# Optimization experiments

Measured on AMD Instinct MI355X. Metric: run time of the kernel, lower is better.

The kernel has to match this reference:

```python
import jax, jax.numpy as jnp
import numpy as np

B, S, H, E, V, T = 64, 256, 1024, 512, 10000, 64
D = H // 2  # per-direction LSTM hidden


def setup_inputs() -> dict:
    key = jax.random.key(0)
    ks = jax.random.split(key, 16)
    s = jnp.float32(0.02)
    emb = jax.random.normal(ks[4], (V, E), jnp.float32) * s
    emb = emb.at[0].set(0.0)  # padding_idx=0
    return {
        "encoder_outputs": jax.random.normal(ks[0], (B, S, H), jnp.float32),
        "enc_h0": jax.random.normal(ks[1], (2, B, D), jnp.float32),
        "enc_c0": jax.random.normal(ks[2], (2, B, D), jnp.float32),
        "target": jax.random.randint(ks[3], (B, T), 1, V),
        "mask": jnp.zeros((B, S), jnp.bool_),
        "sos_idx": 1,
        "emb": emb,
        "Wa": jax.random.normal(ks[5], (H, H), jnp.float32) * s,
        "Ua": jax.random.normal(ks[6], (H, H), jnp.float32) * s,
        "Va": jax.random.normal(ks[7], (H,), jnp.float32) * s,
        "out_W": jax.random.normal(ks[8], (V, H), jnp.float32) * s,
        "out_b": jnp.zeros((V,), jnp.float32),
        "Wih_f": jax.random.normal(ks[9], (4 * D, E + H), jnp.float32) * s,
        "Whh_f": jax.random.normal(ks[10], (4 * D, D), jnp.float32) * s,
        "bih_f": jnp.zeros((4 * D,), jnp.float32),
        "bhh_f": jnp.zeros((4 * D,), jnp.float32),
        "Wih_b": jax.random.normal(ks[11], (4 * D, E + H), jnp.float32) * s,
        "Whh_b": jax.random.normal(ks[12], (4 * D, D), jnp.float32) * s,
        "bih_b": jnp.zeros((4 * D,), jnp.float32),
        "bhh_b": jnp.zeros((4 * D,), jnp.float32),
    }


def _lstm_cell(x, h, c, Wih, Whh, bih, bhh):
    g = x @ Wih.T + h @ Whh.T + bih + bhh
    i, f, gg, o = jnp.split(g, 4, axis=-1)  # torch gate order i,f,g,o
    c2 = jax.nn.sigmoid(f) * c + jax.nn.sigmoid(i) * jnp.tanh(gg)
    h2 = jax.nn.sigmoid(o) * jnp.tanh(c2)
    return h2, c2


def reference(encoder_outputs, enc_h0, enc_c0, target, mask, sos_idx, emb, Wa, Ua, Va,
              out_W, out_b, Wih_f, Whh_f, bih_f, bhh_f, Wih_b, Whh_b, bih_b, bhh_b):
    # Cache Ua(keys) once (original recomputes it each step; math identical).
    Uk = jnp.einsum('bsh,kh->bsk', encoder_outputs, Ua)  # [B,S,H]
    b = encoder_outputs.shape[0]
    tokens = jnp.concatenate(
        [jnp.full((b, 1), sos_idx, target.dtype), target[:, :-1]], axis=1)  # [B,T]
    xs = tokens.T  # [T,B]

    def step(carry, tok):
        h, c = carry  # each [2,B,D]
        query = jnp.swapaxes(h, 0, 1).reshape(b, -1)  # [B,H] (fwd||bwd)
        sc = jnp.einsum('bsh,h->bs', jnp.tanh((query @ Wa.T)[:, None, :] + Uk), Va)
        sc = jnp.where(mask, -jnp.inf, sc)
        w = jax.nn.softmax(sc, axis=-1)  # [B,S]
        ctx = jnp.einsum('bs,bsh->bh', w, encoder_outputs)  # [B,H]
        x = jnp.concatenate([emb[tok], ctx], axis=-1)  # [B,E+H]
        hf, cf = _lstm_cell(x, h[0], c[0], Wih_f, Whh_f, bih_f, bhh_f)
        hb, cb = _lstm_cell(x, h[1], c[1], Wih_b, Whh_b, bih_b, bhh_b)
        out = jnp.concatenate([hf, hb], axis=-1)  # [B,H]
        logits = out @ out_W.T + out_b  # [B,V]
        return (jnp.stack([hf, hb]), jnp.stack([cf, cb])), (logits, w)

    (h, c), (logits, attns) = jax.lax.scan(step, (enc_h0, enc_c0), xs)
    decoder_outputs = jnp.swapaxes(logits, 0, 1)  # [B,T,V]
    attentions = jnp.swapaxes(attns, 0, 1)        # [B,T,S]
    return decoder_outputs, h, c, attentions
```

## Files before the change

kernel.cpp:

```cpp
#include <hip/hip_runtime.h>

#define NB 64
#define NS 256
#define NH 1024
#define NE 512
#define NV 10000
#define NT 64
#define ND 512
#define NEH 1536

typedef __attribute__((ext_vector_type(8))) short bf16x8;
typedef __attribute__((ext_vector_type(4))) float f32x4;

__device__ __forceinline__ short F2B(float f) {
  unsigned u = __float_as_uint(f);
  return (short)((u + 0x7fffu + ((u >> 16) & 1u)) >> 16);
}
__device__ __forceinline__ float B2F(short s) {
  return __uint_as_float(((unsigned)(unsigned short)s) << 16);
}
__device__ __forceinline__ float ftanh(float x) {
  float e = __expf(2.f * x);
  return 1.f - 2.f * __builtin_amdgcn_rcpf(e + 1.f);
}

#define GLD16(src, dst)                                                        \
  __builtin_amdgcn_global_load_lds(                                            \
      (const __attribute__((address_space(1))) void*)(src),                    \
      (__attribute__((address_space(3))) void*)(dst), 16, 0, 0)

__device__ __forceinline__ void mm64_f32a(
    const float* __restrict__ Af, int lda, const short* __restrict__ Wg,
    int ldw, int K, short* Ch, size_t ldc, char* smem)
{
  const int tid = threadIdx.x;
  const int lane = tid & 63, w = tid >> 6;
  const int qm = (w >> 1) << 5, qn = (w & 1) << 5;
  const int kg = lane >> 4, rl = lane & 15;
  f32x4 acc[2][2] = {};
  const int nIt = K >> 6;

  auto stage = [&](int k0, int buf) {
    char* As = smem + (buf << 14);
    char* Bs = As + 8192;
#pragma unroll
    for (int p = 0; p < 2; ++p) {
      int j = tid + (p << 8);
      int row = j >> 3;
      int c = (j & 7) ^ (row & 7);
      const float* src = Af + (size_t)row * lda + k0 + (c << 3);
      float4 v0 = ((const float4*)src)[0];
      float4 v1 = ((const float4*)src)[1];
      bf16x8 pk;
      pk[0] = F2B(v0.x); pk[1] = F2B(v0.y); pk[2] = F2B(v0.z); pk[3] = F2B(v0.w);
      pk[4] = F2B(v1.x); pk[5] = F2B(v1.y); pk[6] = F2B(v1.z); pk[7] = F2B(v1.w);
      *((bf16x8*)As + j) = pk;
    }
#pragma unroll
    for (int p = 0; p < 2; ++p) {
      int j = (w << 7) + (p << 6) + lane;
      int row = j >> 3;
      int c = (j & 7) ^ (row & 7);
      GLD16(Wg + (size_t)row * ldw + k0 + (c << 3), Bs + (w << 11) + (p << 10));
    }
  };

  stage(0, 0);
  for (int it = 0; it < nIt; ++it) {
    __syncthreads();
    if (it + 1 < nIt) stage((it + 1) << 6, (it + 1) & 1);
    const short* As = (const short*)(smem + ((it & 1) << 14));
    const short* Bs = As + 4096;
#pragma unroll
    for (int kk = 0; kk < 2; ++kk) {
      bf16x8 af[2], bfr[2];
#pragma unroll
      for (int mt = 0; mt < 2; ++mt) {
        int r2 = qm + (mt << 4) + rl;
        int c = (kk << 2) + kg;
        af[mt] = *((const bf16x8*)As + ((r2 << 3) | (c ^ (r2 & 7))));
      }
#pragma unroll
      for (int nt = 0; nt < 2; ++nt) {
        int r2 = qn + (nt << 4) + rl;
        int c = (kk << 2) + kg;
        bfr[nt] = *((const bf16x8*)Bs + ((r2 << 3) | (c ^ (r2 & 7))));
      }
#pragma unroll
      for (int mt = 0; mt < 2; ++mt)
#pragma unroll
        for (int nt = 0; nt < 2; ++nt)
          acc[mt][nt] = __builtin_amdgcn_mfma_f32_16x16x32_bf16(
              af[mt], bfr[nt], acc[mt][nt], 0, 0, 0);
    }
  }
#pragma unroll
  for (int mt = 0; mt < 2; ++mt)
#pragma unroll
    for (int nt = 0; nt < 2; ++nt) {
      int cn = qn + (nt << 4) + rl;
#pragma unroll
      for (int r = 0; r < 4; ++r) {
        int rowm = qm + (mt << 4) + (kg << 2) + r;
        Ch[(size_t)rowm * ldc + cn] = F2B(acc[mt][nt][r]);
      }
    }
}

__global__ __launch_bounds__(256) void uk_mm_f32(const float* __restrict__ enc,
                                                 const short* __restrict__ Ua_h,
                                                 short* __restrict__ Uk_h) {
  __shared__ char smem[32768];
  mm64_f32a(enc + (size_t)blockIdx.y * 64 * NH, NH,
            Ua_h + (size_t)blockIdx.x * 64 * NH, NH, NH,
            Uk_h + (size_t)blockIdx.y * 64 * NH + blockIdx.x * 64, NH, smem);
}

template <int MODE>
__global__ __launch_bounds__(256) void mm128(
    const short* __restrict__ A, const short* __restrict__ Bw, int nvmax,
    const float* __restrict__ bias, float* __restrict__ Cf,
    short* __restrict__ Ch)
{
  __shared__ char smem[32768];
  const int tid = threadIdx.x, lane = tid & 63, w = tid >> 6;
  const int m0 = blockIdx.y << 7;
  const int n0 = blockIdx.x << 7;
  const int qm = (w >> 1) << 6, qn = (w & 1) << 6;
  const int kg = lane >> 4, rl = lane & 15;
  f32x4 acc[4][4] = {};
  for (int k0 = 0; k0 < NH; k0 += 64) {
#pragma unroll
    for (int p = 0; p < 4; ++p) {
      int j = (((w << 2) + p) << 6) + lane;
      int row = j >> 3;
      int c = (j & 7) ^ (row & 7);
      GLD16(A + (size_t)(m0 + row) * NH + k0 + (c << 3),
            smem + (((w << 2) + p) << 10));
      int vr = n0 + row; if (vr > nvmax - 1) vr = nvmax - 1;
      GLD16(Bw + (size_t)vr * NH + k0 + (c << 3),
            smem + 16384 + (((w << 2) + p) << 10));
    }
    __syncthreads();
    const short* As = (const short*)smem;
    const short* Bs = (const short*)(smem + 16384);
#pragma unroll
    for (int kk = 0; kk < 2; ++kk) {
      bf16x8 af[4], bfr[4];
#pragma unroll
      for (int mt = 0; mt < 4; ++mt) {
        int r2 = qm + (mt << 4) + rl;
        int c = (kk << 2) + kg;
        af[mt] = *((const bf16x8*)As + ((r2 << 3) | (c ^ (r2 & 7))));
      }
#pragma unroll
      for (int nt = 0; nt < 4; ++nt) {
        int r2 = qn + (nt << 4) + rl;
        int c = (kk << 2) + kg;
        bfr[nt] = *((const bf16x8*)Bs + ((r2 << 3) | (c ^ (r2 & 7))));
      }
#pragma unroll
      for (int mt = 0; mt < 4; ++mt)
#pragma unroll
        for (int nt = 0; nt < 4; ++nt)
          acc[mt][nt] = __builtin_amdgcn_mfma_f32_16x16x32_bf16(
              af[mt], bfr[nt], acc[mt][nt], 0, 0, 0);
    }
    __syncthreads();
  }
#pragma unroll
  for (int nt = 0; nt < 4; ++nt) {
    int colv = n0 + qn + (nt << 4) + rl;
    if (colv < nvmax) {
#pragma unroll
      for (int mt = 0; mt < 4; ++mt)
#pragma unroll
        for (int r = 0; r < 4; ++r) {
          int m = m0 + qm + (mt << 4) + (kg << 2) + r;
          if (MODE == 0) {
            int b = m & 63, t = m >> 6;
            Cf[(size_t)((b << 6) + t) * NV + colv] = acc[mt][nt][r] + bias[colv];
          } else {
            Ch[(size_t)m * NH + colv] = F2B(acc[mt][nt][r]);
          }
        }
    }
  }
}

__global__ __launch_bounds__(256) void gates_v2(
    const short* __restrict__ Xt, const short* __restrict__ hcur,
    const short* __restrict__ Wcomb, const float* __restrict__ bperm,
    const float* __restrict__ cq_old, float* __restrict__ hq_f,
    float* __restrict__ cq_new, short* __restrict__ hnext)
{
  __shared__ char smem[61440];
  const int tid = threadIdx.x, lane = tid & 63, w = tid >> 6;
  const int kg = lane >> 4, rl = lane & 15;
  const int dir = blockIdx.x >> 7, gi = blockIdx.x & 127;
  const int hoff = dir << 9;
  const short* Wbase = Wcomb + (((size_t)(dir << 11) + (gi << 4)) << 11);

  auto stage = [&](int it, int buf) {
    char* dst = smem + buf * 20480;
#pragma unroll
    for (int g = 0; g < 4; ++g) {
      int row = (g << 4) + (w << 2) + kg;
      int c = rl ^ (row & 15);
      int k = (it << 7) + (c << 3);
      const short* src = (k < NEH) ? (Xt + (size_t)row * NEH + k)
                                   : (hcur + (size_t)row * NH + hoff + (k - NEH));
      GLD16(src, dst + (g << 12) + (w << 10));
    }
    {
      int rowB = (w << 2) + kg;
      int cB = rl ^ rowB;
      int kB = (it << 7) + (cB << 3);
      GLD16(Wbase + (size_t)rowB * 2048 + kB, dst + 16384 + (w << 10));
    }
  };

  stage(0, 0); stage(1, 1); stage(2, 2);
  f32x4 acc = {};
// ... 17 lines not shown
    __builtin_amdgcn_sched_barrier(0);
    __builtin_amdgcn_s_barrier();
    if (it + 3 < 16) stage(it + 3, buf);
    buf = (buf == 2) ? 0 : buf + 1;
  }
  float* gacc = (float*)smem;
#pragma unroll
  for (int r = 0; r < 4; ++r)
    gacc[((w << 4) + (kg << 2) + r) * 17 + rl] = acc[r];
  __syncthreads();
  {
    const int b = tid >> 2, j2 = tid & 3;
    const float* bp = bperm + (dir << 11) + (gi << 4) + (j2 << 2);
    const float* gr = gacc + b * 17 + (j2 << 2);
    float gi_ = gr[0] + bp[0];
    float gf_ = gr[1] + bp[1];
    float gg_ = gr[2] + bp[2];
    float go_ = gr[3] + bp[3];
    const int d = ((gi >> 2) << 4) + (((gi << 2) + j2) & 15);
    const int idx = (b << 10) + hoff + d;
    float c0v = cq_old[idx];
    float si = 1.f / (1.f + __expf(-gi_));
    float sf = 1.f / (1.f + __expf(-gf_));
    float so = 1.f / (1.f + __expf(-go_));
    float tg = ftanh(gg_);
    float c2 = sf * c0v + si * tg;
    float h2 = so * ftanh(c2);
    hq_f[idx] = h2;
    cq_new[idx] = c2;
    hnext[idx] = F2B(h2);
  }
}

__global__ __launch_bounds__(256) void q_mm2(const short* __restrict__ hcur,
                                             const short* __restrict__ Wa_h,
                                             float* __restrict__ q)
{
  __shared__ char smem[61440];
  const int tid = threadIdx.x, lane = tid & 63, w = tid >> 6;
  const int kg = lane >> 4, rl = lane & 15;
  const int n0 = blockIdx.x << 4;
  const short* Wbase = Wa_h + (size_t)n0 * NH;

  auto stage = [&](int it, int buf) {
    char* dst = smem + buf * 20480;
#pragma unroll
    for (int g = 0; g < 4; ++g) {
      int row = (g << 4) + (w << 2) + kg;
      int c = rl ^ (row & 15);
      int k = (it << 7) + (c << 3);
      GLD16(hcur + (size_t)row * NH + k, dst + (g << 12) + (w << 10));
    }
    {
      int rowB = (w << 2) + kg;
      int cB = rl ^ rowB;
      int kB = (it << 7) + (cB << 3);
      GLD16(Wbase + (size_t)rowB * NH + kB, dst + 16384 + (w << 10));
    }
  };

  stage(0, 0); stage(1, 1); stage(2, 2);
  f32x4 acc = {};
  int buf = 0;
  for (int it = 0; it < 8; ++it) {
    if (it < 6)       asm volatile("s_waitcnt vmcnt(10)" ::: "memory");
    else if (it == 6) asm volatile("s_waitcnt vmcnt(5)" ::: "memory");
    else              asm volatile("s_waitcnt vmcnt(0)" ::: "memory");
    __builtin_amdgcn_s_barrier();
    __builtin_amdgcn_sched_barrier(0);
    const short* As = (const short*)(smem + buf * 20480);
    const short* Bs = (const short*)(smem + buf * 20480 + 16384);
    const int rowA = (w << 4) + rl;
#pragma unroll
    for (int kk = 0; kk < 4; ++kk) {
      int chunk = (kk << 2) | kg;
      bf16x8 af = *((const bf16x8*)As + ((rowA << 4) | (chunk ^ (rowA & 15))));
      bf16x8 bf = *((const bf16x8*)Bs + ((rl << 4) | (chunk ^ rl)));
      acc = __builtin_amdgcn_mfma_f32_16x16x32_bf16(af, bf, acc, 0, 0, 0);
    }
    __builtin_amdgcn_sched_barrier(0);
    __builtin_amdgcn_s_barrier();
    if (it + 3 < 8) stage(it + 3, buf);
    buf = (buf == 2) ? 0 : buf + 1;
  }
#pragma unroll
  for (int r = 0; r < 4; ++r)
    q[(size_t)((w << 4) + (kg << 2) + r) * NH + n0 + rl] = acc[r];
}

__global__ __launch_bounds__(256) void f2b_k(const float* __restrict__ in,
                                             short* __restrict__ out, int n4) {
  int i = blockIdx.x * 256 + threadIdx.x;
  const int stride = gridDim.x * 256;
  for (; i < n4; i += stride) {
    float4 v = ((const float4*)in)[i];
    short4 o;
    o.x = F2B(v.x); o.y = F2B(v.y); o.z = F2B(v.z); o.w = F2B(v.w);
    ((short4*)out)[i] = o;
  }
}

__global__ __launch_bounds__(256) void perm_w(
    const float* __restrict__ Wih_f, const float* __restrict__ Whh_f,
    const float* __restrict__ Wih_b, const float* __restrict__ Whh_b,
    const float* __restrict__ bih_f, const float* __restrict__ bhh_f,
    const float* __restrict__ bih_b, const float* __restrict__ bhh_b,
    short* __restrict__ Wcomb, float* __restrict__ bias_perm)
{
  int i = blockIdx.x * 256 + threadIdx.x;
  int k4 = i & 511;
  int np = (i >> 9) & 2047;
  int dir = i >> 20;
  int gate = np & 3, dlo = (np >> 2) & 15, dblk = np >> 6;
  int d = (dblk << 4) + dlo;
  int r = (gate << 9) + d;
  int k = k4 << 2;
  const float* Wih = dir ? Wih_b : Wih_f;
  const float* Whh = dir ? Whh_b : Whh_f;
  float4 v = (k < NEH) ? *(const float4*)(Wih + (size_t)r * NEH + k)
                       : *(const float4*)(Whh + (size_t)r * ND + (k - NEH));
  short4 o;
  o.x = F2B(v.x); o.y = F2B(v.y); o.z = F2B(v.z); o.w = F2B(v.w);
  *(short4*)(Wcomb + ((size_t)((dir << 11) + np) << 11) + k) = o;
  if (k4 == 0) {
    const float* bi = dir ? bih_b : bih_f;
    const float* bh = dir ? bhh_b : bhh_f;
    bias_perm[(dir << 11) + np] = bi[r] + bh[r];
  }
}

__global__ __launch_bounds__(256) void emb_fill(
    const float* __restrict__ emb, const int* __restrict__ target,
    const int* __restrict__ sos, short* __restrict__ Xbuf)
{
  int idx = blockIdx.x * 256 + threadIdx.x;
  int t = idx >> 13;
  int r = idx & 8191;
  int b = r >> 7, e4 = r & 127;
  int tok = (t == 0) ? sos[0] : target[b * NT + t - 1];
  float4 v = *(const float4*)(emb + (size_t)tok * NE + (e4 << 2));
  short4 o;
  o.x = F2B(v.x); o.y = F2B(v.y); o.z = F2B(v.z); o.w = F2B(v.w);
  *(short4*)(Xbuf + (size_t)(t * NB + b) * NEH + (e4 << 2)) = o;
}

__global__ __launch_bounds__(256) void init_state(
    const float* __restrict__ h0, const float* __restrict__ c0,
    float* __restrict__ hq, float* __restrict__ cq, short* __restrict__ H0) {
  int idx = blockIdx.x * 256 + threadIdx.x;
  int b = idx >> 10, dir = (idx >> 9) & 1, d = idx & 511;
  int src = dir * NB * ND + (b << 9) + d;
  float h = h0[src];
  hq[idx] = h;
  cq[idx] = c0[src];
  H0[idx] = F2B(h);
}

__global__ __launch_bounds__(256) void final_state(
    const float* __restrict__ hq, const float* __restrict__ cq,
    float* __restrict__ out_h, float* __restrict__ out_c) {
  int idx = blockIdx.x * 256 + threadIdx.x;
  int dir = idx >> 15, r = idx & 32767, b = r >> 9, d = r & 511;
  int src = b * NH + dir * ND + d;
  out_h[idx] = hq[src];
  out_c[idx] = cq[src];
}

__global__ __launch_bounds__(256) void attn_score(
    const float* __restrict__ q, const short* __restrict__ Uk,
    const float* __restrict__ Va, const unsigned char* __restrict__ mask,
    float* __restrict__ sc) {
  __shared__ float qs[NH];
  const int b = blockIdx.x >> 6;
  {
    int t4 = threadIdx.x << 2;
    *(float4*)(qs + t4) = *(const float4*)(q + (size_t)b * NH + t4);
  }
  __syncthreads();
  const int lane = threadIdx.x & 63, wid = threadIdx.x >> 6;
  const int bs = (blockIdx.x << 2) + wid;
  const short* ukp = Uk + (size_t)bs * NH;
  float acc = 0.f;
#pragma unroll
  for (int i = 0; i < 2; ++i) {
    int h = (i << 9) + (lane << 3);
    bf16x8 uv = *(const bf16x8*)(ukp + h);
    float4 q0 = *(const float4*)(qs + h);
    float4 q1 = *(const float4*)(qs + h + 4);
    float4 v0 = *(const float4*)(Va + h);
    float4 v1 = *(const float4*)(Va + h + 4);
    acc += v0.x * ftanh(q0.x + B2F(uv[0]));
    acc += v0.y * ftanh(q0.y + B2F(uv[1]));
    acc += v0.z * ftanh(q0.z + B2F(uv[2]));
    acc += v0.w * ftanh(q0.w + B2F(uv[3]));
    acc += v1.x * ftanh(q1.x + B2F(uv[4]));
    acc += v1.y * ftanh(q1.y + B2F(uv[5]));
    acc += v1.z * ftanh(q1.z + B2F(uv[6]));
    acc += v1.w * ftanh(q1.w + B2F(uv[7]));
  }
#pragma unroll
  for (int o = 32; o; o >>= 1) acc += __shfl_down(acc, o);
  if (lane == 0) sc[bs] = mask[bs] ? -__builtin_inff() : acc;
}

__global__ __launch_bounds__(256) void ctx_soft(
    const float* __restrict__ sc, const float* __restrict__ enc_f,
    const short* __restrict__ enc_h, int use_h,
    short* __restrict__ Xt, float* __restrict__ attn_out, int t) {
  const int tid = threadIdx.x;
  const int b = blockIdx.x >> 2, qh = blockIdx.x & 3;
  __shared__ float red[4];
  __shared__ float ws[NS];
  __shared__ float4 red4[4][64];
  float v = sc[b * NS + tid];
  float m = v;
#pragma unroll
  for (int o = 32; o; o >>= 1) m = fmaxf(m, __shfl_down(m, o));
  if ((tid & 63) == 0) red[tid >> 6] = m;
  __syncthreads();
  m = fmaxf(fmaxf(red[0], red[1]), fmaxf(red[2], red[3]));
  float e = __expf(v - m);
  float su = e;
#pragma unroll
  for (int o = 32; o; o >>= 1) su += __shfl_down(su, o);
  __syncthreads();
  if ((tid & 63) == 0) red[tid >> 6] = su;
  __syncthreads();
  su = red[0] + red[1] + red[2] + red[3];
  float wgt = e / su;
  ws[tid] = wgt;
  if (qh == 0) attn_out[((size_t)b * NT + t) * NS + tid] = wgt;
  __syncthreads();
  const int w = tid >> 6, l = tid & 63;
  const int h = (qh << 8) + (l << 2);
  const int s0 = w << 6;
  float4 a = make_float4(0.f, 0.f, 0.f, 0.f);
  if (use_h) {
    const short* ep = enc_h + ((size_t)b * NS + s0) * NH + h;
    for (int s = 0; s < 64; ++s) {
      short4 vv = *(const short4*)(ep + (size_t)s * NH);
      float wv = ws[s0 + s];
      a.x += wv * B2F(vv.x); a.y += wv * B2F(vv.y);
      a.z += wv * B2F(vv.z); a.w += wv * B2F(vv.w);
    }
  } else {
    const float* ep = enc_f + ((size_t)b * NS + s0) * NH + h;
    for (int s = 0; s < 64; ++s) {
      float4 vv = *(const float4*)(ep + (size_t)s * NH);
      float wv = ws[s0 + s];
      a.x += wv * vv.x; a.y += wv * vv.y; a.z += wv * vv.z; a.w += wv * vv.w;
    }
  }
  red4[w][l] = a;
  __syncthreads();
  if (tid < 64) {
    float4 r0 = red4[0][tid], r1 = red4[1][tid], r2 = red4[2][tid],
           r3 = red4[3][tid];
    short4 o;
    o.x = F2B(r0.x + r1.x + r2.x + r3.x);
    o.y = F2B(r0.y + r1.y + r2.y + r3.y);
    o.z = F2B(r0.z + r1.z + r2.z + r3.z);
    o.w = F2B(r0.w + r1.w + r2.w + r3.w);
    *(short4*)(Xt + (size_t)b * NEH + NE + (qh << 8) + (tid << 2)) = o;
  }
}

extern "C" void kernel_launch(void* const* d_in, const int* in_sizes, int n_in,
                              void* d_out, int out_size, void* d_ws, size_t ws_size,
                              hipStream_t stream)
{
  const float* enc    = (const float*)d_in[0];
  const float* h0     = (const float*)d_in[1];
  const float* c0     = (const float*)d_in[2];
  const int*   target = (const int*)d_in[3];
  const unsigned char* mask = (const unsigned char*)d_in[4];
  const int*   sos    = (const int*)d_in[5];
  const float* emb    = (const float*)d_in[6];
  const float* Wa     = (const float*)d_in[7];
  const float* Ua     = (const float*)d_in[8];
  const float* Va     = (const float*)d_in[9];
  const float* out_W  = (const float*)d_in[10];
  const float* out_b  = (const float*)d_in[11];
  const float* Wih_f  = (const float*)d_in[12];
  const float* Whh_f  = (const float*)d_in[13];
  const float* bih_f  = (const float*)d_in[14];
  const float* bhh_f  = (const float*)d_in[15];
  const float* Wih_b  = (const float*)d_in[16];
  const float* Whh_b  = (const float*)d_in[17];
  const float* bih_b  = (const float*)d_in[18];
  const float* bhh_b  = (const float*)d_in[19];

  float* out_dec  = (float*)d_out;
  float* out_h    = out_dec + (size_t)NB * NT * NV;
  float* out_c    = out_h + 2 * NB * ND;
  float* out_attn = out_c + 2 * NB * ND;

  char* base = (char*)d_ws;
  size_t off = 0;
  auto alloc = [&](size_t bytes) -> char* {
    char* p = base + off;
    off += (bytes + 255) & ~(size_t)255;
    return p;
  };
  short* Uk_h  = (short*)alloc((size_t)NB * NS * NH * 2);
  short* ow_h  = (short*)alloc((size_t)NV * NH * 2);
  short* Ua_h  = (short*)alloc((size_t)NH * NH * 2);
  short* Wa_h  = (short*)alloc((size_t)NH * NH * 2);
  short* Wcomb = (short*)alloc((size_t)2 * 2048 * 2048 * 2);
  float* bperm = (float*)alloc((size_t)2 * 2048 * 4);
  float* q     = (float*)alloc((size_t)NB * NH * 4);
  float* sc    = (float*)alloc((size_t)NB * NS * 4);
  short* Xbuf  = (short*)alloc((size_t)NT * NB * NEH * 2);
  float* hq    = (float*)alloc((size_t)NB * NH * 4);
  float* cq    = (float*)alloc((size_t)2 * NB * NH * 4);
  short* Hbuf  = (short*)alloc((size_t)(NT + 1) * NB * NH * 2);
  short* enc_h = nullptr;
  int use_h = 0;
  if (off + (size_t)NB * NS * NH * 2 <= ws_size) {
    enc_h = (short*)alloc((size_t)NB * NS * NH * 2);
    use_h = 1;
  }
  if (off > ws_size) return;

  f2b_k<<<dim3(2048), dim3(256), 0, stream>>>(out_W, ow_h, NV * NH / 4);
  f2b_k<<<dim3(1024), dim3(256), 0, stream>>>(Ua, Ua_h, NH * NH / 4);
  f2b_k<<<dim3(1024), dim3(256), 0, stream>>>(Wa, Wa_h, NH * NH / 4);
  perm_w<<<dim3(8192), dim3(256), 0, stream>>>(Wih_f, Whh_f, Wih_b, Whh_b,
                                               bih_f, bhh_f, bih_b, bhh_b,
                                               Wcomb, bperm);
  emb_fill<<<dim3(2048), dim3(256), 0, stream>>>(emb, target, sos, Xbuf);
  init_state<<<dim3(256), dim3(256), 0, stream>>>(h0, c0, hq, cq, Hbuf);
  if (use_h) {
    f2b_k<<<dim3(2048), dim3(256), 0, stream>>>(enc, enc_h, NB * NS * NH / 4);
    mm128<1><<<dim3(8, 128), dim3(256), 0, stream>>>(enc_h, Ua_h, NH, nullptr,
                                                     nullptr, Uk_h);
  } else {
    uk_mm_f32<<<dim3(16, 256), dim3(256), 0, stream>>>(enc, Ua_h, Uk_h);
  }

  for (int t = 0; t < NT; ++t) {
    const short* hcur = Hbuf + (size_t)t * NB * NH;
    short* hnext = Hbuf + (size_t)(t + 1) * NB * NH;
    float* cq_cur = cq + (t & 1) * (NB * NH);
    float* cq_nxt = cq + ((t & 1) ^ 1) * (NB * NH);
    short* Xt = Xbuf + (size_t)t * NB * NEH;

    q_mm2<<<dim3(64), dim3(256), 0, stream>>>(hcur, Wa_h, q);
    attn_score<<<dim3(4096), dim3(256), 0, stream>>>(q, Uk_h, Va, mask, sc);
    ctx_soft<<<dim3(256), dim3(256), 0, stream>>>(sc, enc, enc_h, use_h,
                                                  Xt, out_attn, t);
    gates_v2<<<dim3(256), dim3(256), 0, stream>>>(Xt, hcur, Wcomb, bperm,
                                                  cq_cur, hq, cq_nxt, hnext);
  }

  mm128<0><<<dim3(79, 32), dim3(256), 0, stream>>>(Hbuf + NB * NH, ow_h, NV,
                                                   out_b, out_dec, nullptr);
  final_state<<<dim3(256), dim3(256), 0, stream>>>(hq, cq, out_h, out_c);
}
```

Baseline: 2.095 ms.

## Fuse query projection with attention scoring using transposed Uk layout

Measured after the change: 3.331 ms. +59.0%, slower.

```diff
diff --git a/kernel.cpp b/kernel.cpp
--- a/kernel.cpp
+++ b/kernel.cpp
@@ -29,166 +29,130 @@
       (const __attribute__((address_space(1))) void*)(src),                    \
       (__attribute__((address_space(3))) void*)(dst), 16, 0, 0)
 
-__device__ __forceinline__ void mm64_f32a(
-    const float* __restrict__ Af, int lda, const short* __restrict__ Wg,
-    int ldw, int K, short* Ch, size_t ldc, char* smem)
-{
+__device__ __forceinline__ size_t ukt_idx(int b, int s, int h) {
+  return ((((size_t)b * 128 + (h >> 3)) << 8) + s) * 8 + (h & 7);
+}
+
+__global__ __launch_bounds__(256) void score_q(
+    const short* __restrict__ Hcur,
+    const short* __restrict__ Wp,
+    const short* __restrict__ UkT,
+    const float* __restrict__ Va,
+    float* __restrict__ psc)
+{
+  __shared__ float hs[NH];
+  __shared__ float qs[256];
+  __shared__ float vs[256];
   const int tid = threadIdx.x;
-  const int lane = tid & 63, w = tid >> 6;
-  const int qm = (w >> 1) << 5, qn = (w & 1) << 5;
-  const int kg = lane >> 4, rl = lane & 15;
-  f32x4 acc[2][2] = {};
-  const int nIt = K >> 6;
-
-  auto stage = [&](int k0, int buf) {
-    char* As = smem + (buf << 14);
-    char* Bs = As + 8192;
-#pragma unroll
-    for (int p = 0; p < 2; ++p) {
-      int j = tid + (p << 8);
-      int row = j >> 3;
-      int c = (j & 7) ^ (row & 7);
-      const float* src = Af + (size_t)row * lda + k0 + (c << 3);
-      float4 v0 = ((const float4*)src)[0];
-      float4 v1 = ((const float4*)src)[1];
-      bf16x8 pk;
-      pk[0] = F2B(v0.x); pk[1] = F2B(v0.y); pk[2] = F2B(v0.z); pk[3] = F2B(v0.w);
-      pk[4] = F2B(v1.x); pk[5] = F2B(v1.y); pk[6] = F2B(v1.z); pk[7] = F2B(v1.w);
-      *((bf16x8*)As + j) = pk;
-    }
-#pragma unroll
-    for (int p = 0; p < 2; ++p) {
-      int j = (w << 7) + (p << 6) + lane;
-      int row = j >> 3;
-      int c = (j & 7) ^ (row & 7);
-      GLD16(Wg + (size_t)row * ldw + k0 + (c << 3), Bs + (w << 11) + (p << 10));
-    }
-  };
-
-  stage(0, 0);
-  for (int it = 0; it < nIt; ++it) {
-    __syncthreads();
-    if (it + 1 < nIt) stage((it + 1) << 6, (it + 1) & 1);
-    const short* As = (const short*)(smem + ((it & 1) << 14));
-    const short* Bs = As + 4096;
-#pragma unroll
-    for (int kk = 0; kk < 2; ++kk) {
-      bf16x8 af[2], bfr[2];
-#pragma unroll
-      for (int mt = 0; mt < 2; ++mt) {
-        int r2 = qm + (mt << 4) + rl;
-        int c = (kk << 2) + kg;
-        af[mt] = *((const bf16x8*)As + ((r2 << 3) | (c ^ (r2 & 7))));
-      }
-#pragma unroll
-      for (int nt = 0; nt < 2; ++nt) {
-        int r2 = qn + (nt << 4) + rl;
-        int c = (kk << 2) + kg;
-        bfr[nt] = *((const bf16x8*)Bs + ((r2 << 3) | (c ^ (r2 & 7))));
-      }
-#pragma unroll
-      for (int mt = 0; mt < 2; ++mt)
-#pragma unroll
-        for (int nt = 0; nt < 2; ++nt)
-          acc[mt][nt] = __builtin_amdgcn_mfma_f32_16x16x32_bf16(
-              af[mt], bfr[nt], acc[mt][nt], 0, 0, 0);
-    }
-  }
-#pragma unroll
-  for (int mt = 0; mt < 2; ++mt)
-#pragma unroll
-    for (int nt = 0; nt < 2; ++nt) {
-      int cn = qn + (nt << 4) + rl;
-#pragma unroll
-      for (int r = 0; r < 4; ++r) {
-        int rowm = qm + (mt << 4) + (kg << 2) + r;
-        Ch[(size_t)rowm * ldc + cn] = F2B(acc[mt][nt][r]);
-      }
-    }
-}
-
-__global__ __launch_bounds__(256) void uk_mm_f32(const float* __restrict__ enc,
-                                                 const short* __restrict__ Ua_h,
-                                                 short* __restrict__ Uk_h) {
-  __shared__ char smem[32768];
-  mm64_f32a(enc + (size_t)blockIdx.y * 64 * NH, NH,
-            Ua_h + (size_t)blockIdx.x * 64 * NH, NH, NH,
-            Uk_h + (size_t)blockIdx.y * 64 * NH + blockIdx.x * 64, NH, smem);
-}
-
-template <int MODE>
-__global__ __launch_bounds__(256) void mm128(
-    const short* __restrict__ A, const short* __restrict__ Bw, int nvmax,
-    const float* __restrict__ bias, float* __restrict__ Cf,
-    short* __restrict__ Ch)
-{
-  __shared__ char smem[32768];
-  const int tid = threadIdx.x, lane = tid & 63, w = tid >> 6;
-  const int m0 = blockIdx.y << 7;
-  const int n0 = blockIdx.x << 7;
-  const int qm = (w >> 1) << 6, qn = (w & 1) << 6;
-  const int kg = lane >> 4, rl = lane & 15;
-  f32x4 acc[4][4] = {};
-  for (int k0 = 0; k0 < NH; k0 += 64) {
-#pragma unroll
-    for (int p = 0; p < 4; ++p) {
-      int j = (((w << 2) + p) << 6) + lane;
-      int row = j >> 3;
-      int c = (j & 7) ^ (row & 7);
-      GLD16(A + (size_t)(m0 + row) * NH + k0 + (c << 3),
-            smem + (((w << 2) + p) << 10));
-      int vr = n0 + row; if (vr > nvmax - 1) vr = nvmax - 1;
-      GLD16(Bw + (size_t)vr * NH + k0 + (c << 3),
-            smem + 16384 + (((w << 2) + p) << 10));
-    }
-    __syncthreads();
-    const short* As = (const short*)smem;
-    const short* Bs = (const short*)(smem + 16384);
-#pragma unroll
-    for (int kk = 0; kk < 2; ++kk) {
-      bf16x8 af[4], bfr[4];
-#pragma unroll
-      for (int mt = 0; mt < 4; ++mt) {
-        int r2 = qm + (mt << 4) + rl;
-        int c = (kk << 2) + kg;
-        af[mt] = *((const bf16x8*)As + ((r2 << 3) | (c ^ (r2 & 7))));
-      }
-#pragma unroll
-      for (int nt = 0; nt < 4; ++nt) {
-        int r2 = qn + (nt << 4) + rl;
-        int c = (kk << 2) + kg;
-        bfr[nt] = *((const bf16x8*)Bs + ((r2 << 3) | (c ^ (r2 & 7))));
-      }
-#pragma unroll
-      for (int mt = 0; mt < 4; ++mt)
-#pragma unroll
-        for (int nt = 0; nt < 4; ++nt)
-          acc[mt][nt] = __builtin_amdgcn_mfma_f32_16x16x32_bf16(
-              af[mt], bfr[nt], acc[mt][nt], 0, 0, 0);
-    }
-    __syncthreads();
-  }
-#pragma unroll
-  for (int nt = 0; nt < 4; ++nt) {
-    int colv = n0 + qn + (nt << 4) + rl;
-    if (colv < nvmax) {
-#pragma unroll
-      for (int mt = 0; mt < 4; ++mt)
-#pragma unroll
-        for (int r = 0; r < 4; ++r) {
-          int m = m0 + qm + (mt << 4) + (kg << 2) + r;
-          if (MODE == 0) {
-            int b = m & 63, t = m >> 6;
-            Cf[(size_t)((b << 6) + t) * NV + colv] = acc[mt][nt][r] + bias[colv];
-          } else {
-            Ch[(size_t)m * NH + colv] = F2B(acc[mt][nt][r]);
-          }
-        }
-    }
-  }
-}
-
-__global__ __launch_bounds__(256) void gates_v2(
+  const int b = blockIdx.x >> 2, hq = blockIdx.x & 3;
+
+  {
+    short4 hv = *(const short4*)(Hcur + b * NH + (tid << 2));
+    hs[(tid << 2) + 0] = B2F(hv.x);
+    hs[(tid << 2) + 1] = B2F(hv.y);
+    hs[(tid << 2) + 2] = B2F(hv.z);
+    hs[(tid << 2) + 3] = B2F(hv.w);
+    vs[tid] = Va[(hq << 8) + tid];
+  }
+  __syncthreads();
+
+  {
+    const int n = (hq << 8) + tid;
+    float acc = 0.f;
+#pragma unroll 4
+    for (int k8 = 0; k8 < 128; ++k8) {
+      bf16x8 wv = *((const bf16x8*)Wp + ((size_t)k8 << 10) + n);
+      const float* hp = hs + (k8 << 3);
+#pragma unroll
+      for (int j = 0; j < 8; ++j) acc += hp[j] * B2F(wv[j]);
+    }
+    qs[tid] = acc;
+  }
+  __syncthreads();
+
+  {
+    float a = 0.f;
+    const bf16x8* up = (const bf16x8*)UkT +
+                       (((size_t)b * 128 + (hq << 5)) << 8) + tid;
+#pragma unroll 1
+    for (int h8 = 0; h8 < 32; ++h8) {
+      bf16x8 uv = up[(size_t)h8 << 8];
+      const float* qp = qs + (h8 << 3);
+      const float* vp = vs + (h8 << 3);
+#pragma unroll
+      for (int j = 0; j < 8; ++j)
+        a += vp[j] * ftanh(qp[j] + B2F(uv[j]));
+    }
+    psc[(((hq) << 6) + b) * 256 + tid] = a;
+  }
+}
+
+__global__ __launch_bounds__(256) void ctx_soft2(
+    const float* __restrict__ psc, const unsigned char* __restrict__ mask,
+    const short* __restrict__ enc_h, const float* __restrict__ enc_f,
+    int use_h, short* __restrict__ Xt, float* __restrict__ attn_out, int t)
+{
+  const int tid = threadIdx.x;
+  const int b = blockIdx.x >> 2, qh = blockIdx.x & 3;
+  __shared__ float red[4];
+  __shared__ float ws[NS];
+  __shared__ float4 red4[256];
+  float v = psc[(b << 8) + tid] + psc[(64 + b) * 256 + tid] +
+            psc[(128 + b) * 256 + tid] + psc[(192 + b) * 256 + tid];
+  if (mask[(b << 8) + tid]) v = -__builtin_inff();
+  float m = v;
+#pragma unroll
+  for (int o = 32; o; o >>= 1) m = fmaxf(m, __shfl_down(m, o));
+  if ((tid & 63) == 0) red[tid >> 6] = m;
+  __syncthreads();
+  m = fmaxf(fmaxf(red[0], red[1]), fmaxf(red[2], red[3]));
+  float e = __expf(v - m);
+  float su = e;
+#pragma unroll
+  for (int o = 32; o; o >>= 1) su += __shfl_down(su, o);
+  __syncthreads();
+  if ((tid & 63) == 0) red[tid >> 6] = su;
+  __syncthreads();
+  su = red[0] + red[1] + red[2] + red[3];
+  float wgt = e / su;
+  ws[tid] = wgt;
+  if (qh == 0) attn_out[((size_t)b * NT + t) * NS + tid] = wgt;
+  __syncthreads();
+  const int w = tid >> 6, l = tid & 63;
+  const int h = (qh << 8) + (l << 2);
+  const int s0 = w << 6;
+  float4 a = make_float4(0.f, 0.f, 0.f, 0.f);
+  if (use_h) {
+    const short* ep = enc_h + ((size_t)b * NS + s0) * NH + h;
+    for (int s = 0; s < 64; ++s) {
+      short4 vv = *(const short4*)(ep + (size_t)s * NH);
+      float wv = ws[s0 + s];
+      a.x += wv * B2F(vv.x); a.y += wv * B2F(vv.y);
+      a.z += wv * B2F(vv.z); a.w += wv * B2F(vv.w);
+    }
+  } else {
+    const float* ep = enc_f + ((size_t)b * NS + s0) * NH + h;
+    for (int s = 0; s < 64; ++s) {
+      float4 vv = *(const float4*)(ep + (size_t)s * NH);
+      float wv = ws[s0 + s];
+      a.x += wv * vv.x; a.y += wv * vv.y; a.z += wv * vv.z; a.w += wv * vv.w;
+    }
+  }
+  red4[(w << 6) + l] = a;
+  __syncthreads();
+  if (tid < 64) {
+    float4 r0 = red4[tid], r1 = red4[64 + tid], r2 = red4[128 + tid],
+           r3 = red4[192 + tid];
+    short4 o;
+    o.x = F2B(r0.x + r1.x + r2.x + r3.x);
+    o.y = F2B(r0.y + r1.y + r2.y + r3.y);
+    o.z = F2B(r0.z + r1.z + r2.z + r3.z);
+    o.w = F2B(r0.w + r1.w + r2.w + r3.w);
+    *(short4*)(Xt + (size_t)b * NEH + NE + (qh << 8) + (tid << 2)) = o;
+  }
+}
+
+__global__ __launch_bounds__(256) void gates_k(
     const short* __restrict__ Xt, const short* __restrict__ hcur,
     const short* __restrict__ Wcomb, const float* __restrict__ bperm,
     const float* __restrict__ cq_old, float* __restrict__ hq_f,
@@ -272,60 +236,159 @@
   }
 }
 
-__global__ __launch_bounds__(256) void q_mm2(const short* __restrict__ hcur,
-                                             const short* __restrict__ Wa_h,
-                                             float* __restrict__ q)
-{
-  __shared__ char smem[61440];
+__global__ __launch_bounds__(256) void uk_mm_f32(const float* __restrict__ enc,
+                                                 const short* __restrict__ Ua_h,
+                                                 short* __restrict__ UkT) {
+  __shared__ char smem[32768];
+  const float* Af = enc + (size_t)blockIdx.y * 64 * NH;
+  const short* Wg = Ua_h + (size_t)blockIdx.x * 64 * NH;
+  const int m0 = blockIdx.y * 64, c0 = blockIdx.x * 64;
+  const int tid = threadIdx.x;
+  const int lane = tid & 63, w = tid >> 6;
+  const int qm = (w >> 1) << 5, qn = (w & 1) << 5;
+  const int kg = lane >> 4, rl = lane & 15;
+  f32x4 acc[2][2] = {};
+
+  auto stage = [&](int k0, int buf) {
+    char* As = smem + (buf << 14);
+    char* Bs = As + 8192;
+#pragma unroll
+    for (int p = 0; p < 2; ++p) {
+      int j = tid + (p << 8);
+      int row = j >> 3;
+      int c = (j & 7) ^ (row & 7);
+      const float* src = Af + (size_t)row * NH + k0 + (c << 3);
+      float4 v0 = ((const float4*)src)[0];
+      float4 v1 = ((const float4*)src)[1];
+      bf16x8 pk;
+      pk[0] = F2B(v0.x); pk[1] = F2B(v0.y); pk[2] = F2B(v0.z); pk[3] = F2B(v0.w);
+      pk[4] = F2B(v1.x); pk[5] = F2B(v1.y); pk[6] = F2B(v1.z); pk[7] = F2B(v1.w);
+      *((bf16x8*)As + j) = pk;
+    }
+#pragma unroll
+    for (int p = 0; p < 2; ++p) {
+      int j = (w << 7) + (p << 6) + lane;
+      int row = j >> 3;
+      int c = (j & 7) ^ (row & 7);
+      GLD16(Wg + (size_t)row * NH + k0 + (c << 3), Bs + (w << 11) + (p << 10));
+    }
+  };
+
+  stage(0, 0);
+  for (int it = 0; it < 16; ++it) {
+    __syncthreads();
+    if (it + 1 < 16) stage((it + 1) << 6, (it + 1) & 1);
+    const short* As = (const short*)(smem + ((it & 1) << 14));
+    const short* Bs = As + 4096;
+#pragma unroll
+    for (int kk = 0; kk < 2; ++kk) {
+      bf16x8 af[2], bfr[2];
+#pragma unroll
+      for (int mt = 0; mt < 2; ++mt) {
+        int r2 = qm + (mt << 4) + rl;
+        int c = (kk << 2) + kg;
+        af[mt] = *((const bf16x8*)As + ((r2 << 3) | (c ^ (r2 & 7))));
+      }
+#pragma unroll
+      for (int nt = 0; nt < 2; ++nt) {
+        int r2 = qn + (nt << 4) + rl;
+        int c = (kk << 2) + kg;
+        bfr[nt] = *((const bf16x8*)Bs + ((r2 << 3) | (c ^ (r2 & 7))));
+      }
+#pragma unroll
+      for (int mt = 0; mt < 2; ++mt)
+#pragma unroll
+        for (int nt = 0; nt < 2; ++nt)
+          acc[mt][nt] = __builtin_amdgcn_mfma_f32_16x16x32_bf16(
+              af[mt], bfr[nt], acc[mt][nt], 0, 0, 0);
+    }
+  }
+#pragma unroll
+  for (int mt = 0; mt < 2; ++mt)
+#pragma unroll
+    for (int nt = 0; nt < 2; ++nt) {
+      int cn = qn + (nt << 4) + rl;
+#pragma unroll
+      for (int r = 0; r < 4; ++r) {
+        int m = m0 + qm + (mt << 4) + (kg << 2) + r;
+        int h = c0 + cn;
+        UkT[ukt_idx(m >> 8, m & 255, h)] = F2B(acc[mt][nt][r]);
+      }
+    }
+}
+
+template <int MODE>
+__global__ __launch_bounds__(256) void mm128(
+    const short* __restrict__ A, const short* __restrict__ Bw, int nvmax,
+    const float* __restrict__ bias, float* __restrict__ Cf,
+    short* __restrict__ Ch, int ntm)
+{
+  __shared__ char smem[32768];
   const int tid = threadIdx.x, lane = tid & 63, w = tid >> 6;
+  const int chunk = gridDim.x >> 3;
+  const int swz = (blockIdx.x & 7) * chunk + (blockIdx.x >> 3);
+  const int m0 = (swz % ntm) << 7;
+  const int n0 = (swz / ntm) << 7;
+  const int qm = (w >> 1) << 6, qn = (w & 1) << 6;
   const int kg = lane >> 4, rl = lane & 15;
-  const int n0 = blockIdx.x << 4;
-  const short* Wbase = Wa_h + (size_t)n0 * NH;
-
-  auto stage = [&](int it, int buf) {
-    char* dst = smem + buf * 20480;
-#pragma unroll
-    for (int g = 0; g < 4; ++g) {
-      int row = (g << 4) + (w << 2) + kg;
-      int c = rl ^ (row & 15);
-      int k = (it << 7) + (c << 3);
-      GLD16(hcur + (size_t)row * NH + k, dst + (g << 12) + (w << 10));
-    }
-    {
-      int rowB = (w << 2) + kg;
-      int cB = rl ^ rowB;
-      int kB = (it << 7) + (cB << 3);
-      GLD16(Wbase + (size_t)rowB * NH + kB, dst + 16384 + (w << 10));
-    }
-  };
-
-  stage(0, 0); stage(1, 1); stage(2, 2);
-  f32x4 acc = {};
-  int buf = 0;
-  for (int it = 0; it < 8; ++it) {
-    if (it < 6)       asm volatile("s_waitcnt vmcnt(10)" ::: "memory");
-    else if (it == 6) asm volatile("s_waitcnt vmcnt(5)" ::: "memory");
-    else              asm volatile("s_waitcnt vmcnt(0)" ::: "memory");
-    __builtin_amdgcn_s_barrier();
-    __builtin_amdgcn_sched_barrier(0);
-    const short* As = (const short*)(smem + buf * 20480);
-    const short* Bs = (const short*)(smem + buf * 20480 + 16384);
-    const int rowA = (w << 4) + rl;
-#pragma unroll
-    for (int kk = 0; kk < 4; ++kk) {
-      int chunk = (kk << 2) | kg;
-      bf16x8 af = *((const bf16x8*)As + ((rowA << 4) | (chunk ^ (rowA & 15))));
-      bf16x8 bf = *((const bf16x8*)Bs + ((rl << 4) | (chunk ^ rl)));
-      acc = __builtin_amdgcn_mfma_f32_16x16x32_bf16(af, bf, acc, 0, 0, 0);
-    }
-    __builtin_amdgcn_sched_barrier(0);
-    __builtin_amdgcn_s_barrier();
-    if (it + 3 < 8) stage(it + 3, buf);
-    buf = (buf == 2) ? 0 : buf + 1;
-  }
-#pragma unroll
-  for (int r = 0; r < 4; ++r)
-    q[(size_t)((w << 4) + (kg << 2) + r) * NH + n0 + rl] = acc[r];
+  f32x4 acc[4][4] = {};
+  for (int k0 = 0; k0 < NH; k0 += 64) {
+#pragma unroll
+    for (int p = 0; p < 4; ++p) {
+      int j = (((w << 2) + p) << 6) + lane;
+      int row = j >> 3;
+      int c = (j & 7) ^ (row & 7);
+      GLD16(A + (size_t)(m0 + row) * NH + k0 + (c << 3),
+            smem + (((w << 2) + p) << 10));
+      int vr = n0 + row; if (vr > nvmax - 1) vr = nvmax - 1;
+      GLD16(Bw + (size_t)vr * NH + k0 + (c << 3),
+            smem + 16384 + (((w << 2) + p) << 10));
+    }
+    __syncthreads();
+    const short* As = (const short*)smem;
+    const short* Bs = (const short*)(smem + 16384);
+#pragma unroll
+    for (int kk = 0; kk < 2; ++kk) {
+      bf16x8 af[4], bfr[4];
+#pragma unroll
+      for (int mt = 0; mt < 4; ++mt) {
+        int r2 = qm + (mt << 4) + rl;
+        int c = (kk << 2) + kg;
+        af[mt] = *((const bf16x8*)As + ((r2 << 3) | (c ^ (r2 & 7))));
+      }
+#pragma unroll
+      for (int nt = 0; nt < 4; ++nt) {
+        int r2 = qn + (nt << 4) + rl;
+        int c = (kk << 2) + kg;
+        bfr[nt] = *((const bf16x8*)Bs + ((r2 << 3) | (c ^ (r2 & 7))));
+      }
+#pragma unroll
+      for (int mt = 0; mt < 4; ++mt)
+#pragma unroll
+        for (int nt = 0; nt < 4; ++nt)
+          acc[mt][nt] = __builtin_amdgcn_mfma_f32_16x16x32_bf16(
+              af[mt], bfr[nt], acc[mt][nt], 0, 0, 0);
+    }
+    __syncthreads();
+  }
+#pragma unroll
+  for (int nt = 0; nt < 4; ++nt) {
+    int colv = n0 + qn + (nt << 4) + rl;
+    if (colv < nvmax) {
+#pragma unroll
+      for (int mt = 0; mt < 4; ++mt)
+#pragma unroll
+        for (int r = 0; r < 4; ++r) {
+          int m = m0 + qm + (mt << 4) + (kg << 2) + r;
+          if (MODE == 0) {
+            int b = m & 63, t = m >> 6;
+            Cf[(size_t)((b << 6) + t) * NV + colv] = acc[mt][nt][r] + bias[colv];
+          } else {
+            Ch[ukt_idx(m >> 8, m & 255, colv)] = F2B(acc[mt][nt][r]);
+          }
+        }
+    }
+  }
 }
 
 __global__ __launch_bounds__(256) void f2b_k(const float* __restrict__ in,
@@ -338,6 +401,17 @@
     o.x = F2B(v.x); o.y = F2B(v.y); o.z = F2B(v.z); o.w = F2B(v.w);
     ((short4*)out)[i] = o;
   }
+}
+
+__global__ __launch_bounds__(256) void wp_pack(const float* __restrict__ Wa,
+                                               short* __restrict__ Wp) {
+  int i = blockIdx.x * 256 + threadIdx.x;
+  int k8 = i >> 10, n = i & 1023;
+  const float* src = Wa + (size_t)n * NH + (k8 << 3);
+  bf16x8 o;
+#pragma unroll
+  for (int j = 0; j < 8; ++j) o[j] = F2B(src[j]);
+  *((bf16x8*)Wp + i) = o;
 }
 
 __global__ __launch_bounds__(256) void perm_w(
@@ -404,105 +478,6 @@
   int src = b * NH + dir * ND + d;
   out_h[idx] = hq[src];
   out_c[idx] = cq[src];
-}
-
-__global__ __launch_bounds__(256) void attn_score(
-    const float* __restrict__ q, const short* __restrict__ Uk,
-    const float* __restrict__ Va, const unsigned char* __restrict__ mask,
-    float* __restrict__ sc) {
-  __shared__ float qs[NH];
-  const int b = blockIdx.x >> 6;
-  {
-    int t4 = threadIdx.x << 2;
-    *(float4*)(qs + t4) = *(const float4*)(q + (size_t)b * NH + t4);
-  }
-  __syncthreads();
-  const int lane = threadIdx.x & 63, wid = threadIdx.x >> 6;
-  const int bs = (blockIdx.x << 2) + wid;
-  const short* ukp = Uk + (size_t)bs * NH;
-  float acc = 0.f;
-#pragma unroll
-  for (int i = 0; i < 2; ++i) {
-    int h = (i << 9) + (lane << 3);
-    bf16x8 uv = *(const bf16x8*)(ukp + h);
-    float4 q0 = *(const float4*)(qs + h);
-    float4 q1 = *(const float4*)(qs + h + 4);
-    float4 v0 = *(const float4*)(Va + h);
-    float4 v1 = *(const float4*)(Va + h + 4);
-    acc += v0.x * ftanh(q0.x + B2F(uv[0]));
-    acc += v0.y * ftanh(q0.y + B2F(uv[1]));
-    acc += v0.z * ftanh(q0.z + B2F(uv[2]));
-    acc += v0.w * ftanh(q0.w + B2F(uv[3]));
-    acc += v1.x * ftanh(q1.x + B2F(uv[4]));
-    acc += v1.y * ftanh(q1.y + B2F(uv[5]));
-    acc += v1.z * ftanh(q1.z + B2F(uv[6]));
-    acc += v1.w * ftanh(q1.w + B2F(uv[7]));
-  }
-#pragma unroll
-  for (int o = 32; o; o >>= 1) acc += __shfl_down(acc, o);
-  if (lane == 0) sc[bs] = mask[bs] ? -__builtin_inff() : acc;
-}
-
-__global__ __launch_bounds__(256) void ctx_soft(
-    const float* __restrict__ sc, const float* __restrict__ enc_f,
-    const short* __restrict__ enc_h, int use_h,
-    short* __restrict__ Xt, float* __restrict__ attn_out, int t) {
-  const int tid = threadIdx.x;
-  const int b = blockIdx.x >> 2, qh = blockIdx.x & 3;
-  __shared__ float red[4];
-  __shared__ float ws[NS];
-  __shared__ float4 red4[4][64];
-  float v = sc[b * NS + tid];
-  float m = v;
-#pragma unroll
-  for (int o = 32; o; o >>= 1) m = fmaxf(m, __shfl_down(m, o));
-  if ((tid & 63) == 0) red[tid >> 6] = m;
-  __syncthreads();
-  m = fmaxf(fmaxf(red[0], red[1]), fmaxf(red[2], red[3]));
-  float e = __expf(v - m);
-  float su = e;
-#pragma unroll
-  for (int o = 32; o; o >>= 1) su += __shfl_down(su, o);
-  __syncthreads();
-  if ((tid & 63) == 0) red[tid >> 6] = su;
-  __syncthreads();
-  su = red[0] + red[1] + red[2] + red[3];
-  float wgt = e / su;
-  ws[tid] = wgt;
-  if (qh == 0) attn_out[((size_t)b * NT + t) * NS + tid] = wgt;
-  __syncthreads();
-  const int w = tid >> 6, l = tid & 63;
-  const int h = (qh << 8) + (l << 2);
-  const int s0 = w << 6;
-  float4 a = make_float4(0.f, 0.f, 0.f, 0.f);
-  if (use_h) {
-    const short* ep = enc_h + ((size_t)b * NS + s0) * NH + h;
-    for (int s = 0; s < 64; ++s) {
-      short4 vv = *(const short4*)(ep + (size_t)s * NH);
-      float wv = ws[s0 + s];
-      a.x += wv * B2F(vv.x); a.y += wv * B2F(vv.y);
-      a.z += wv * B2F(vv.z); a.w += wv * B2F(vv.w);
-    }
-  } else {
-    const float* ep = enc_f + ((size_t)b * NS + s0) * NH + h;
-    for (int s = 0; s < 64; ++s) {
-      float4 vv = *(const float4*)(ep + (size_t)s * NH);
-      float wv = ws[s0 + s];
-      a.x += wv * vv.x; a.y += wv * vv.y; a.z += wv * vv.z; a.w += wv * vv.w;
-    }
-  }
-  red4[w][l] = a;
-  __syncthreads();
-  if (tid < 64) {
-    float4 r0 = red4[0][tid], r1 = red4[1][tid], r2 = red4[2][tid],
-           r3 = red4[3][tid];
-    short4 o;
-    o.x = F2B(r0.x + r1.x + r2.x + r3.x);
-    o.y = F2B(r0.y + r1.y + r2.y + r3.y);
-    o.z = F2B(r0.z + r1.z + r2.z + r3.z);
-    o.w = F2B(r0.w + r1.w + r2.w + r3.w);
-    *(short4*)(Xt + (size_t)b * NEH + NE + (qh << 8) + (tid << 2)) = o;
-  }
 }
 
 extern "C" void kernel_launch(void* const* d_in, const int* in_sizes, int n_in,
@@ -542,14 +517,13 @@
     off += (bytes + 255) & ~(size_t)255;
     return p;
   };
-  short* Uk_h  = (short*)alloc((size_t)NB * NS * NH * 2);
+  short* UkT   = (short*)alloc((size_t)NB * NS * NH * 2);
   short* ow_h  = (short*)alloc((size_t)NV * NH * 2);
   short* Ua_h  = (short*)alloc((size_t)NH * NH * 2);
-  short* Wa_h  = (short*)alloc((size_t)NH * NH * 2);
+  short* Wp    = (short*)alloc((size_t)NH * NH * 2);
   short* Wcomb = (short*)alloc((size_t)2 * 2048 * 2048 * 2);
   float* bperm = (float*)alloc((size_t)2 * 2048 * 4);
-  float* q     = (float*)alloc((size_t)NB * NH * 4);
-  float* sc    = (float*)alloc((size_t)NB * NS * 4);
+  float* psc   = (float*)alloc((size_t)4 * NB * NS * 4);
   short* Xbuf  = (short*)alloc((size_t)NT * NB * NEH * 2);
   float* hq    = (float*)alloc((size_t)NB * NH * 4);
   float* cq    = (float*)alloc((size_t)2 * NB * NH * 4);
@@ -564,7 +538,7 @@
 
   f2b_k<<<dim3(2048), dim3(256), 0, stream>>>(out_W, ow_h, NV * NH / 4);
   f2b_k<<<dim3(1024), dim3(256), 0, stream>>>(Ua, Ua_h, NH * NH / 4);
-  f2b_k<<<dim3(1024), dim3(256), 0, stream>>>(Wa, Wa_h, NH * NH / 4);
+  wp_pack<<<dim3(512), dim3(256), 0, stream>>>(Wa, Wp);
   perm_w<<<dim3(8192), dim3(256), 0, stream>>>(Wih_f, Whh_f, Wih_b, Whh_b,
                                                bih_f, bhh_f, bih_b, bhh_b,
                                                Wcomb, bperm);
@@ -572,10 +546,10 @@
   init_state<<<dim3(256), dim3(256), 0, stream>>>(h0, c0, hq, cq, Hbuf);
   if (use_h) {
     f2b_k<<<dim3(2048), dim3(256), 0, stream>>>(enc, enc_h, NB * NS * NH / 4);
-    mm128<1><<<dim3(8, 128), dim3(256), 0, stream>>>(enc_h, Ua_h, NH, nullptr,
-                                                     nullptr, Uk_h);
+    mm128<1><<<dim3(1024), dim3(256), 0, stream>>>(enc_h, Ua_h, NH, nullptr,
+                                                   nullptr, UkT, 128);
   } else {
-    uk_mm_f32<<<dim3(16, 256), dim3(256), 0, stream>>>(enc, Ua_h, Uk_h);
+    uk_mm_f32<<<dim3(16, 256), dim3(256), 0, stream>>>(enc, Ua_h, UkT);
   }
 
   for (int t = 0; t < NT; ++t) {
@@ -585,15 +559,14 @@
     float* cq_nxt = cq + ((t & 1) ^ 1) * (NB * NH);
     short* Xt = Xbuf + (size_t)t * NB * NEH;
 
-    q_mm2<<<dim3(64), dim3(256), 0, stream>>>(hcur, Wa_h, q);
-    attn_score<<<dim3(4096), dim3(256), 0, stream>>>(q, Uk_h, Va, mask, sc);
-    ctx_soft<<<dim3(256), dim3(256), 0, stream>>>(sc, enc, enc_h, use_h,
-                                                  Xt, out_attn, t);
-    gates_v2<<<dim3(256), dim3(256), 0, stream>>>(Xt, hcur, Wcomb, bperm,
-                                                  cq_cur, hq, cq_nxt, hnext);
-  }
-
-  mm128<0><<<dim3(79, 32), dim3(256), 0, stream>>>(Hbuf + NB * NH, ow_h, NV,
-                                                   out_b, out_dec, nullptr);
+    score_q<<<dim3(256), dim3(256), 0, stream>>>(hcur, Wp, UkT, Va, psc);
+    ctx_soft2<<<dim3(256), dim3(256), 0, stream>>>(psc, mask, enc_h, enc,
+                                                   use_h, Xt, out_attn, t);
+    gates_k<<<dim3(256), dim3(256), 0, stream>>>(Xt, hcur, Wcomb, bperm,
+                                                 cq_cur, hq, cq_nxt, hnext);
+  }
+
+  mm128<0><<<dim3(2528), dim3(256), 0, stream>>>(Hbuf + NB * NH, ow_h, NV,
+                                                 out_b, out_dec, nullptr, 32);
   final_state<<<dim3(256), dim3(256), 0, stream>>>(hq, cq, out_h, out_c);
 }
```

## Double-buffer GEMM LDS staging and widen ctx_soft to 512 threads

Applied to the files above, without the earlier changes.

Result: no change. 2.104 ms (+0.4%).

```diff
diff --git a/kernel.cpp b/kernel.cpp
--- a/kernel.cpp
+++ b/kernel.cpp
@@ -117,33 +117,43 @@
 }
 
 template <int MODE>
-__global__ __launch_bounds__(256) void mm128(
+__global__ __launch_bounds__(256) void mm128p(
     const short* __restrict__ A, const short* __restrict__ Bw, int nvmax,
     const float* __restrict__ bias, float* __restrict__ Cf,
     short* __restrict__ Ch)
 {
-  __shared__ char smem[32768];
+  __shared__ char smem[65536];
   const int tid = threadIdx.x, lane = tid & 63, w = tid >> 6;
   const int m0 = blockIdx.y << 7;
   const int n0 = blockIdx.x << 7;
   const int qm = (w >> 1) << 6, qn = (w & 1) << 6;
   const int kg = lane >> 4, rl = lane & 15;
   f32x4 acc[4][4] = {};
-  for (int k0 = 0; k0 < NH; k0 += 64) {
+
+  auto stage = [&](int it, int buf) {
+    char* dst = smem + (buf << 15);
+    const int k0 = it << 6;
 #pragma unroll
     for (int p = 0; p < 4; ++p) {
       int j = (((w << 2) + p) << 6) + lane;
       int row = j >> 3;
       int c = (j & 7) ^ (row & 7);
       GLD16(A + (size_t)(m0 + row) * NH + k0 + (c << 3),
-            smem + (((w << 2) + p) << 10));
+            dst + (((w << 2) + p) << 10));
       int vr = n0 + row; if (vr > nvmax - 1) vr = nvmax - 1;
       GLD16(Bw + (size_t)vr * NH + k0 + (c << 3),
-            smem + 16384 + (((w << 2) + p) << 10));
-    }
-    __syncthreads();
-    const short* As = (const short*)smem;
-    const short* Bs = (const short*)(smem + 16384);
+            dst + 16384 + (((w << 2) + p) << 10));
+    }
+  };
+
+  stage(0, 0); stage(1, 1);
+  for (int it = 0; it < 16; ++it) {
+    if (it < 15) asm volatile("s_waitcnt vmcnt(8)" ::: "memory");
+    else         asm volatile("s_waitcnt vmcnt(0)" ::: "memory");
+    __builtin_amdgcn_s_barrier();
+    __builtin_amdgcn_sched_barrier(0);
+    const short* As = (const short*)(smem + ((it & 1) << 15));
+    const short* Bs = As + 8192;
 #pragma unroll
     for (int kk = 0; kk < 2; ++kk) {
       bf16x8 af[4], bfr[4];
@@ -166,7 +176,9 @@
           acc[mt][nt] = __builtin_amdgcn_mfma_f32_16x16x32_bf16(
               af[mt], bfr[nt], acc[mt][nt], 0, 0, 0);
     }
-    __syncthreads();
+    __builtin_amdgcn_sched_barrier(0);
+    __builtin_amdgcn_s_barrier();
+    if (it + 2 < 16) stage(it + 2, it & 1);
   }
 #pragma unroll
   for (int nt = 0; nt < 4; ++nt) {
@@ -443,22 +455,24 @@
   if (lane == 0) sc[bs] = mask[bs] ? -__builtin_inff() : acc;
 }
 
-__global__ __launch_bounds__(256) void ctx_soft(
-    const float* __restrict__ sc, const float* __restrict__ enc_f,
-    const short* __restrict__ enc_h, int use_h,
+__global__ __launch_bounds__(512) void ctx_soft(
+    const float* __restrict__ sc, const short* __restrict__ enc_h,
+    const float* __restrict__ enc_f, int use_h,
     short* __restrict__ Xt, float* __restrict__ attn_out, int t) {
   const int tid = threadIdx.x;
   const int b = blockIdx.x >> 2, qh = blockIdx.x & 3;
-  __shared__ float red[4];
+  __shared__ float red[8];
   __shared__ float ws[NS];
-  __shared__ float4 red4[4][64];
-  float v = sc[b * NS + tid];
+  __shared__ float4 red4[512];
+  const int s8 = tid & 255;
+  float v = sc[b * NS + s8];
   float m = v;
 #pragma unroll
   for (int o = 32; o; o >>= 1) m = fmaxf(m, __shfl_down(m, o));
   if ((tid & 63) == 0) red[tid >> 6] = m;
   __syncthreads();
-  m = fmaxf(fmaxf(red[0], red[1]), fmaxf(red[2], red[3]));
+  m = fmaxf(fmaxf(fmaxf(red[0], red[1]), fmaxf(red[2], red[3])),
+            fmaxf(fmaxf(red[4], red[5]), fmaxf(red[6], red[7])));
   float e = __expf(v - m);
   float su = e;
 #pragma unroll
@@ -468,16 +482,16 @@
   __syncthreads();
   su = red[0] + red[1] + red[2] + red[3];
   float wgt = e / su;
-  ws[tid] = wgt;
-  if (qh == 0) attn_out[((size_t)b * NT + t) * NS + tid] = wgt;
+  ws[s8] = wgt;
+  if (qh == 0 && tid < 256) attn_out[((size_t)b * NT + t) * NS + tid] = wgt;
   __syncthreads();
-  const int w = tid >> 6, l = tid & 63;
+  const int w8 = tid >> 6, l = tid & 63;
   const int h = (qh << 8) + (l << 2);
-  const int s0 = w << 6;
+  const int s0 = w8 << 5;
   float4 a = make_float4(0.f, 0.f, 0.f, 0.f);
   if (use_h) {
     const short* ep = enc_h + ((size_t)b * NS + s0) * NH + h;
-    for (int s = 0; s < 64; ++s) {
+    for (int s = 0; s < 32; ++s) {
       short4 vv = *(const short4*)(ep + (size_t)s * NH);
       float wv = ws[s0 + s];
       a.x += wv * B2F(vv.x); a.y += wv * B2F(vv.y);
@@ -485,22 +499,23 @@
     }
   } else {
     const float* ep = enc_f + ((size_t)b * NS + s0) * NH + h;
-    for (int s = 0; s < 64; ++s) {
+    for (int s = 0; s < 32; ++s) {
       float4 vv = *(const float4*)(ep + (size_t)s * NH);
       float wv = ws[s0 + s];
       a.x += wv * vv.x; a.y += wv * vv.y; a.z += wv * vv.z; a.w += wv * vv.w;
     }
   }
-  red4[w][l] = a;
+  red4[(w8 << 6) + l] = a;
   __syncthreads();
   if (tid < 64) {
-    float4 r0 = red4[0][tid], r1 = red4[1][tid], r2 = red4[2][tid],
-           r3 = red4[3][tid];
+    float sx = 0.f, sy = 0.f, sz = 0.f, sw = 0.f;
+#pragma unroll
+    for (int k = 0; k < 8; ++k) {
+      float4 r = red4[(k << 6) + tid];
+      sx += r.x; sy += r.y; sz += r.z; sw += r.w;
+    }
     short4 o;
-    o.x = F2B(r0.x + r1.x + r2.x + r3.x);
-    o.y = F2B(r0.y + r1.y + r2.y + r3.y);
-    o.z = F2B(r0.z + r1.z + r2.z + r3.z);
-    o.w = F2B(r0.w + r1.w + r2.w + r3.w);
+    o.x = F2B(sx); o.y = F2B(sy); o.z = F2B(sz); o.w = F2B(sw);
     *(short4*)(Xt + (size_t)b * NEH + NE + (qh << 8) + (tid << 2)) = o;
   }
 }
@@ -572,8 +587,8 @@
   init_state<<<dim3(256), dim3(256), 0, stream>>>(h0, c0, hq, cq, Hbuf);
   if (use_h) {
     f2b_k<<<dim3(2048), dim3(256), 0, stream>>>(enc, enc_h, NB * NS * NH / 4);
-    mm128<1><<<dim3(8, 128), dim3(256), 0, stream>>>(enc_h, Ua_h, NH, nullptr,
-                                                     nullptr, Uk_h);
+    mm128p<1><<<dim3(8, 128), dim3(256), 0, stream>>>(enc_h, Ua_h, NH, nullptr,
+                                                      nullptr, Uk_h);
   } else {
     uk_mm_f32<<<dim3(16, 256), dim3(256), 0, stream>>>(enc, Ua_h, Uk_h);
   }
@@ -587,13 +602,13 @@
 
     q_mm2<<<dim3(64), dim3(256), 0, stream>>>(hcur, Wa_h, q);
     attn_score<<<dim3(4096), dim3(256), 0, stream>>>(q, Uk_h, Va, mask, sc);
-    ctx_soft<<<dim3(256), dim3(256), 0, stream>>>(sc, enc, enc_h, use_h,
+    ctx_soft<<<dim3(256), dim3(512), 0, stream>>>(sc, enc_h, enc, use_h,
                                                   Xt, out_attn, t);
     gates_v2<<<dim3(256), dim3(256), 0, stream>>>(Xt, hcur, Wcomb, bperm,
                                                   cq_cur, hq, cq_nxt, hnext);
   }
 
-  mm128<0><<<dim3(79, 32), dim3(256), 0, stream>>>(Hbuf + NB * NH, ow_h, NV,
-                                                   out_b, out_dec, nullptr);
+  mm128p<0><<<dim3(79, 32), dim3(256), 0, stream>>>(Hbuf + NB * NH, ow_h, NV,
+                                                    out_b, out_dec, nullptr);
   final_state<<<dim3(256), dim3(256), 0, stream>>>(hq, cq, out_h, out_c);
 }
```
